# Kernel tuning notes

Measured on AMD Instinct MI355X. Metric: run time of the kernel, lower is better.

The kernel has to match this reference:

```python
import jax, jax.numpy as jnp
import numpy as np

EMBED, IN_DIM, HID, LAYERS, NVIEW = 1024, 256, 256, 3, 6


def _lstm_layer(x_seq, Wih, Whh, bih, bhh):
    # x_seq: [BM, N, D]; torch LSTM gate order i,f,g,o
    BM = x_seq.shape[0]
    h0 = jnp.zeros((BM, HID), x_seq.dtype)
    c0 = jnp.zeros((BM, HID), x_seq.dtype)

    def step(carry, x_t):
        h, c = carry
        gates = x_t @ Wih.T + bih + h @ Whh.T + bhh  # [BM, 4H]
        i, f, g, o = jnp.split(gates, 4, axis=-1)
        c = jax.nn.sigmoid(f) * c + jax.nn.sigmoid(i) * jnp.tanh(g)
        h = jax.nn.sigmoid(o) * jnp.tanh(c)
        return (h, c), h

    _, ys = jax.lax.scan(step, (h0, c0), jnp.swapaxes(x_seq, 0, 1))
    return jnp.swapaxes(ys, 0, 1)  # [BM, N, H]


def setup_inputs() -> dict:
    key = jax.random.key(0)
    ks = jax.random.split(key, 16)
    B, M = 32, 256
    s = lambda fan: 1.0 / np.sqrt(fan)
    inp = {
        "b_x_swin": jax.random.normal(ks[0], (B, M, NVIEW, EMBED), jnp.float32),
        "b_x_conv": jax.random.normal(ks[1], (B, M, NVIEW, EMBED), jnp.float32),
        "Wc": jax.random.uniform(ks[2], (EMBED, EMBED), jnp.float32, -s(EMBED), s(EMBED)),
        "bc": jax.random.uniform(ks[3], (EMBED,), jnp.float32, -s(EMBED), s(EMBED)),
        "Win": jax.random.uniform(ks[4], (IN_DIM, EMBED), jnp.float32, -s(EMBED), s(EMBED)),
        "b_in": jax.random.uniform(ks[5], (IN_DIM,), jnp.float32, -s(EMBED), s(EMBED)),
        "Wih": jax.random.uniform(ks[6], (LAYERS, 4 * HID, IN_DIM), jnp.float32, -s(HID), s(HID)),
        "Whh": jax.random.uniform(ks[7], (LAYERS, 4 * HID, HID), jnp.float32, -s(HID), s(HID)),
        "bih": jax.random.uniform(ks[8], (LAYERS, 4 * HID), jnp.float32, -s(HID), s(HID)),
        "bhh": jax.random.uniform(ks[9], (LAYERS, 4 * HID), jnp.float32, -s(HID), s(HID)),
        "Wv": jax.random.uniform(ks[10], (1, HID), jnp.float32, -s(HID), s(HID)),
        "bv": jax.random.uniform(ks[11], (1,), jnp.float32, -s(HID), s(HID)),
        "Ws": jax.random.uniform(ks[12], (1, NVIEW), jnp.float32, -s(NVIEW), s(NVIEW)),
        "bs": jax.random.uniform(ks[13], (1,), jnp.float32, -s(NVIEW), s(NVIEW)),
    }
    return inp


def reference(b_x_swin, b_x_conv, Wc, bc, Win, b_in, Wih, Whh, bih, bhh, Wv, bv, Ws, bs):
    B, M, N, C = b_x_swin.shape
    # fc_conv + exact GELU + residual (vectorized over all samples; same math as per-sample loop)
    x = b_x_swin + jax.nn.gelu(b_x_conv @ Wc.T + bc, approximate=False)
    x = x @ Win.T + b_in                         # [B, M, N, IN_DIM]
    x = x.reshape(B * M, N, IN_DIM)              # LSTM batch = B*M, seq = N
    for l in range(LAYERS):
        x = _lstm_layer(x, Wih[l], Whh[l], bih[l], bhh[l])
    v = (x @ Wv.T + bv).reshape(B, M, N)         # fc_viewport + flatten(1)
    score = (v @ Ws.T + bs).squeeze(-1)          # fc_score -> [B, M]
    return jnp.mean(score, axis=1)               # torch.mean per sample -> [B]
```

## Files before the change

### kernel.cpp

```cpp
#include <hip/hip_runtime.h>
#include <math.h>
#include <stdint.h>

typedef unsigned short u16;
typedef float f32x4 __attribute__((ext_vector_type(4)));
typedef short bf16x8 __attribute__((ext_vector_type(8)));

#define NVIEW 6

__device__ __forceinline__ u16 f2bf(float f){
  unsigned u = __float_as_uint(f);
  u += 0x7FFFu + ((u >> 16) & 1u);
  return (u16)(u >> 16);
}
__device__ __forceinline__ float bf2f(u16 h){
  return __uint_as_float(((unsigned)h) << 16);
}
__device__ __forceinline__ float fsig(float x){
  x = fminf(fmaxf(x, -30.f), 30.f);
  return 1.0f / (1.0f + __expf(-x));
}
__device__ __forceinline__ float ftanh(float x){
  x = fminf(fmaxf(x, -15.f), 15.f);
  float e = __expf(2.0f * x);
  return (e - 1.0f) / (e + 1.0f);
}
__device__ __forceinline__ void gload16(const u16* g, u16* l){
  __builtin_amdgcn_global_load_lds((const __attribute__((address_space(1))) unsigned int*)g,
                                   (__attribute__((address_space(3))) unsigned int*)l,
                                   16, 0, 0);
}

__global__ void k_cvt(const float* __restrict__ in, u16* __restrict__ out, long n4){
  long i = (long)blockIdx.x * blockDim.x + threadIdx.x;
  long stride = (long)gridDim.x * blockDim.x;
  for (; i < n4; i += stride){
    const float4 v = ((const float4*)in)[i];
    ushort4 o;
    o.x = f2bf(v.x); o.y = f2bf(v.y); o.z = f2bf(v.z); o.w = f2bf(v.w);
    ((ushort4*)out)[i] = o;
  }
}

__global__ void k_build_wl(const float* __restrict__ Wih, const float* __restrict__ Whh,
                           u16* __restrict__ Wl){
  int idx = blockIdx.x * 256 + threadIdx.x;
  int l   = idx >> 19;
  int rem = idx & 524287;
  int ro  = rem >> 9;
  int k   = rem & 511;
  int u = ro >> 2, q = ro & 3;
  int ri = q * 256 + u;
  float v = (k < 256) ? Wih[(l * 1024 + ri) * 256 + k]
                      : Whh[(l * 1024 + ri) * 256 + (k - 256)];
  Wl[idx] = f2bf(v);
}

__global__ void k_build_bias(const float* __restrict__ bih, const float* __restrict__ bhh,
                             float* __restrict__ biasL, u16* __restrict__ zbuf){
  int idx = blockIdx.x * 256 + threadIdx.x;
  if (idx < 3072){
    int l = idx >> 10; int ro = idx & 1023;
    int u = ro >> 2, q = ro & 3;
    int ri = q * 256 + u;
    biasL[idx] = bih[l * 1024 + ri] + bhh[l * 1024 + ri];
  }
  if (idx < 256) zbuf[idx] = 0;
}

#define DSR(dst, addr) asm volatile("ds_read_b128 %0, %1" : "=v"(dst) : "v"(addr))
#define VM4 asm volatile("s_waitcnt vmcnt(4)" ::: "memory")
#define VM0 asm volatile("s_waitcnt vmcnt(0)" ::: "memory")

template<int EPI>
__global__ __launch_bounds__(512, 2)
void gemm8p(const u16* __restrict__ A, long sA,
            const u16* __restrict__ Bm, long sB,
            int N, int K,
            const float* __restrict__ bias,
            const float* __restrict__ resid,
            u16* __restrict__ outb)
{
  __shared__ __align__(128) u16 shA[2 * 16384];
  __shared__ __align__(128) u16 shB[2 * 16384];

  const int tid  = threadIdx.x;
  const int lane = tid & 63;
  const int wv   = tid >> 6;
  const int wm   = wv >> 2;
  const int wn   = wv & 3;
  const int wm16 = wm * 16, wn16 = wn * 16;
  const int l15  = lane & 15, lk = lane >> 4;
  const int w2   = wv * 2;

  const int nwg = gridDim.x;
  const int qq  = nwg >> 3;
  const int b   = blockIdx.x;
  const int swz = (b & 7) * qq + (b >> 3);
  const int NB  = N >> 8;
  const long m0 = (long)(swz / NB) * 256;
  const int  n0 = (swz % NB) * 256;

  const int NT  = K >> 6;
  const int NIT = NT >> 1;

  const long laneA = (long)(lane >> 3) * sA + (long)(((lane & 7) ^ (lane >> 3)) << 3);
  const long laneB = (long)(lane >> 3) * sB + (long)(((lane & 7) ^ (lane >> 3)) << 3);

  auto STA = [&](int buf, int mh, int t){
    #pragma unroll
    for (int j = 0; j < 2; ++j){
      const int chunk = w2 + j;
      gload16(A + (m0 + mh * 128 + chunk * 8) * sA + (long)t * 64 + laneA,
              shA + buf * 16384 + mh * 8192 + chunk * 512 + lane * 8);
    }
  };
  auto STB = [&](int buf, int nh, int t){
    #pragma unroll
    for (int j = 0; j < 2; ++j){
      const int chunk = w2 + j;
      gload16(Bm + (long)(n0 + nh * 128 + chunk * 8) * sB + (long)t * 64 + laneB,
              shB + buf * 16384 + nh * 8192 + chunk * 512 + lane * 8);
    }
  };

  const unsigned ldsA = (unsigned)(uintptr_t)&shA[0];
  const unsigned ldsB = (unsigned)(uintptr_t)&shB[0];
  const unsigned aAr  = ldsA + (unsigned)((wm16 + l15) * 128 + ((lk ^ (l15 & 7)) << 4));
  const unsigned aBr  = ldsB + (unsigned)((wn16 + l15) * 128 + ((lk ^ (l15 & 7)) << 4));

  f32x4 acc[8][4];
  #pragma unroll
  for (int i = 0; i < 8; ++i)
    #pragma unroll
    for (int j = 0; j < 4; ++j)
      acc[i][j] = (f32x4){0.f, 0.f, 0.f, 0.f};

  STA(0, 0, 0); STB(0, 0, 0); STA(0, 1, 0); STB(0, 1, 0);
  STA(1, 0, 1); STB(1, 1, 1);
  VM4;
  __builtin_amdgcn_s_barrier();

#define PH(BUF, MH, NH, STG, VM)                                              \
  {                                                                           \
    bf16x8 af[2][4], bq[2][2];                                                \
    const unsigned bA  = aAr + ((BUF) * 32768 + (MH) * 16384);                \
    const unsigned bAx = bA ^ 64;                                             \
    const unsigned bB  = aBr + ((BUF) * 32768 + (NH) * 16384);                \
    const unsigned bBx = bB ^ 64;                                             \
    _Pragma("unroll") for (int i = 0; i < 4; ++i){                            \
      DSR(af[0][i], bA  + i * 4096);                                          \
      DSR(af[1][i], bAx + i * 4096);                                          \
    }                                                                         \
    _Pragma("unroll") for (int j = 0; j < 2; ++j){                            \
      DSR(bq[0][j], bB  + j * 8192);                                          \
      DSR(bq[1][j], bBx + j * 8192);                                          \
    }                                                                         \
    STG;                                                                      \
    __builtin_amdgcn_s_barrier();                                             \
    asm volatile("s_waitcnt lgkmcnt(0)" ::: "memory");                        \
    __builtin_amdgcn_sched_barrier(0);     \
    __builtin_amdgcn_s_setprio(1);                                            \
    _Pragma("unroll") for (int i = 0; i < 4; ++i)                             \
      _Pragma("unroll") for (int j = 0; j < 2; ++j)                           \
        _Pragma("unroll") for (int ks = 0; ks < 2; ++ks)                      \
          acc[(MH)*4 + i][(NH)*2 + j] = __builtin_amdgcn_mfma_f32_16x16x32_bf16( \
              af[ks][i], bq[ks][j], acc[(MH)*4 + i][(NH)*2 + j], 0, 0, 0);    \
    __builtin_amdgcn_s_setprio(0);                                            \
    VM;                                                                       \
    __builtin_amdgcn_s_barrier();                                             \
  }

  for (int it = 0; it < NIT - 1; ++it){
    const int t1 = 2 * it + 1;
    PH(0, 0, 0, STB(1, 0, t1),     (void)0);
    PH(0, 1, 0, STA(1, 1, t1),     (void)0);
    PH(0, 0, 1, STB(0, 0, t1 + 1), (void)0);
    PH(0, 1, 1, STA(0, 0, t1 + 1), VM4);
    PH(1, 0, 0, STA(0, 1, t1 + 1), (void)0);
    PH(1, 0, 1, STB(0, 1, t1 + 1), (void)0);
    PH(1, 1, 1, STA(1, 0, t1 + 2), (void)0);
    PH(1, 1, 0, STB(1, 1, t1 + 2), VM4);
  }
  {
    const int t1 = NT - 1;
    PH(0, 0, 0, STB(1, 0, t1), (void)0);
    PH(0, 1, 0, STA(1, 1, t1), (void)0);
    PH(0, 0, 1, (void)0,       (void)0);
    PH(0, 1, 1, (void)0,       VM0);
    PH(1, 0, 0, (void)0,       (void)0);
    PH(1, 0, 1, (void)0,       (void)0);
    PH(1, 1, 1, (void)0,       (void)0);
    PH(1, 1, 0, (void)0,       (void)0);
  }
#undef PH

  #pragma unroll
  for (int mf = 0; mf < 8; ++mf){
    #pragma unroll
    for (int nf = 0; nf < 4; ++nf){
      const int n = n0 + nf * 64 + wn16 + l15;
      const float bz = bias[n];
      const long mrow = m0 + mf * 32 + wm16 + lk * 4;
      #pragma unroll
      for (int r = 0; r < 4; ++r){
        float v = acc[mf][nf][r] + bz;
        const long off = (mrow + r) * (long)N + n;
        if (EPI == 0){
          float ge = 0.5f * v * (1.0f + erff(v * 0.70710678118654752f));
          v = ge + resid[off];
        }
        outb[off] = f2bf(v);
      }
    }
  }
}

template<int EPI>
__global__ __launch_bounds__(256)
void gemm_bt(const u16* __restrict__ A0, long sA0,
             const u16* __restrict__ A1, long sA1, int K0,
             const u16* __restrict__ Bm,
             int N, int K,
             const float* __restrict__ bias,
             const float* __restrict__ resid,
             u16* __restrict__ outb,
             float* __restrict__ cbuf,
             int tstep)
{
  __shared__ __align__(16) u16 lA[128 * 64];
  __shared__ __align__(16) u16 lB[128 * 64];

  const int tid  = threadIdx.x;
  const int lane = tid & 63;
  const int wid  = tid >> 6;
  const int wm = wid >> 1, wn = wid & 1;
  const int l15 = lane & 15, lk = lane >> 4;
  const long m0 = (long)blockIdx.x * 128;
  const int  n0 = blockIdx.y * 128;

  f32x4 acc[4][4];
  #pragma unroll
  for (int i = 0; i < 4; ++i)
    #pragma unroll
    for (int j = 0; j < 4; ++j)
      acc[i][j] = (f32x4){0.f, 0.f, 0.f, 0.f};

  const int rowL = tid >> 3;
  const int col8 = (tid & 7) * 8;

  for (int kt = 0; kt < (K >> 6); ++kt){
    const int kbase = kt << 6;
    #pragma unroll
    for (int c = 0; c < 4; ++c){
      int r = c * 32 + rowL;
      int k = kbase + col8;
      const u16* src = (k < K0) ? (A0 + (m0 + r) * sA0 + k)
                                : (A1 + (m0 + r) * sA1 + (k - K0));
      gload16(src, &lA[r * 64 + col8]);
    }
    #pragma unroll
    for (int c = 0; c < 4; ++c){
      int r = c * 32 + rowL;
      int k = kbase + col8;
      gload16(Bm + (long)(n0 + r) * K + k, &lB[r * 64 + col8]);
    }
    __syncthreads();

    #pragma unroll
    for (int ks = 0; ks < 2; ++ks){
      bf16x8 af[4], bfr[4];
      #pragma unroll
      for (int mf = 0; mf < 4; ++mf)
        af[mf] = *(const bf16x8*)&lA[(wm * 64 + mf * 16 + l15) * 64 + ks * 32 + lk * 8];
      #pragma unroll
      for (int nf = 0; nf < 4; ++nf)
        bfr[nf] = *(const bf16x8*)&lB[(wn * 64 + nf * 16 + l15) * 64 + ks * 32 + lk * 8];
      #pragma unroll
      for (int mf = 0; mf < 4; ++mf)
        #pragma unroll
        for (int nf = 0; nf < 4; ++nf)
          acc[mf][nf] = __builtin_amdgcn_mfma_f32_16x16x32_bf16(af[mf], bfr[nf], acc[mf][nf], 0, 0, 0);
    }
    __syncthreads();
  }

  if (EPI == 0 || EPI == 1){
    #pragma unroll
    for (int mf = 0; mf < 4; ++mf){
      #pragma unroll
      for (int nf = 0; nf < 4; ++nf){
        int  n    = n0 + wn * 64 + nf * 16 + l15;
        long mrow = m0 + wm * 64 + mf * 16 + lk * 4;
        float bz = bias[n];
        #pragma unroll
        for (int r = 0; r < 4; ++r){
          float v = acc[mf][nf][r] + bz;
          long off = (mrow + r) * N + n;
          if (EPI == 0){
            float ge = 0.5f * v * (1.0f + erff(v * 0.70710678118654752f));
            v = ge + resid[off];
          }
          outb[off] = f2bf(v);
        }
      }
    }
  } else {
    const int a  = lane & 3;
    const int qb = lane & ~3;
    #pragma unroll
    for (int mf = 0; mf < 4; ++mf){
      #pragma unroll
      for (int nf = 0; nf < 4; ++nf){
        int n = n0 + wn * 64 + nf * 16 + l15;
        float bz = bias[n];
        float v0 = acc[mf][nf][0] + bz;
        float v1 = acc[mf][nf][1] + bz;
        float v2 = acc[mf][nf][2] + bz;
        float v3 = acc[mf][nf][3] + bz;
        float s0 = (a == 0) ? v0 : (a == 1) ? v1 : (a == 2) ? v2 : v3;
        float s1 = (a == 0) ? v1 : (a == 1) ? v2 : (a == 2) ? v3 : v0;
        float s2 = (a == 0) ? v2 : (a == 1) ? v3 : (a == 2) ? v0 : v1;
        float s3 = (a == 0) ? v3 : (a == 1) ? v0 : (a == 2) ? v1 : v2;
        float r0 = s0;
        float r1 = __shfl(s1, qb + ((a + 3) & 3));
        float r2 = __shfl(s2, qb + ((a + 2) & 3));
        float r3 = __shfl(s3, qb + ((a + 1) & 3));
        float wi = (a == 0) ? r0 : (a == 1) ? r1 : (a == 2) ? r2 : r3;
        float wf = (a == 1) ? r0 : (a == 2) ? r1 : (a == 3) ? r2 : r3;
        float wg = (a == 2) ? r0 : (a == 3) ? r1 : (a == 0) ? r2 : r3;
        float wo = (a == 3) ? r0 : (a == 0) ? r1 : (a == 1) ? r2 : r3;
        long row = m0 + wm * 64 + mf * 16 + lk * 4 + a;
        int  u   = ((n0 + wn * 64 + nf * 16) >> 2) + (l15 >> 2);
        float c_old = (tstep == 0) ? 0.0f : cbuf[row * 256 + u];
        float ii = fsig(wi), ff = fsig(wf), gg = ftanh(wg), oo = fsig(wo);
        float cn = ff * c_old + ii * gg;
        float hn = oo * ftanh(cn);
        cbuf[row * 256 + u] = cn;
        outb[(row * NVIEW + tstep) * 256 + u] = f2bf(hn);
      }
    }
  }
}

__global__ void k_score(const u16* __restrict__ X3, const float* __restrict__ Wv,
                        const float* __restrict__ bv, const float* __restrict__ Ws,
                        const float* __restrict__ bs, float* __restrict__ score){
  int lane = threadIdx.x & 63;
  int bm = blockIdx.x * 4 + (threadIdx.x >> 6);
  const u16* row = X3 + (long)bm * (NVIEW * 256);
  float4 wv = *(const float4*)(Wv + lane * 4);
  float p = 0.f;
  #pragma unroll
  for (int n = 0; n < NVIEW; ++n){
    ushort4 xv = *(const ushort4*)(row + n * 256 + lane * 4);
    float d = bf2f(xv.x) * wv.x + bf2f(xv.y) * wv.y + bf2f(xv.z) * wv.z + bf2f(xv.w) * wv.w;
    p += Ws[n] * d;
  }
  #pragma unroll
  for (int off = 32; off; off >>= 1) p += __shfl_xor(p, off);
  if (lane == 0){
    float sw = Ws[0] + Ws[1] + Ws[2] + Ws[3] + Ws[4] + Ws[5];
    score[bm] = p + bv[0] * sw + bs[0];
  }
}

__global__ void k_mean(const float* __restrict__ score, float* __restrict__ out){
  __shared__ float red[256];
  int b = blockIdx.x, tid = threadIdx.x;
  red[tid] = score[b * 256 + tid];
  __syncthreads();
  for (int s = 128; s > 0; s >>= 1){
    if (tid < s) red[tid] += red[tid + s];
    __syncthreads();
  }
  if (tid == 0) out[b] = red[0] * (1.0f / 256.0f);
}

extern "C" void kernel_launch(void* const* d_in, const int* in_sizes, int n_in,
                              void* d_out, int out_size, void* d_ws, size_t ws_size,
                              hipStream_t stream){
  const float* swin = (const float*)d_in[0];
  const float* conv = (const float*)d_in[1];
  const float* Wc   = (const float*)d_in[2];
  const float* bc   = (const float*)d_in[3];
  const float* Win  = (const float*)d_in[4];
  const float* b_in = (const float*)d_in[5];
  const float* Wih  = (const float*)d_in[6];
  const float* Whh  = (const float*)d_in[7];
  const float* bih  = (const float*)d_in[8];
  const float* bhh  = (const float*)d_in[9];
  const float* Wv   = (const float*)d_in[10];
  const float* bv   = (const float*)d_in[11];
  const float* Ws   = (const float*)d_in[12];
  const float* bs   = (const float*)d_in[13];
  float* out = (float*)d_out;

  char* w = (char*)d_ws;
  u16*  convb = (u16*)(w);
  u16*  X0    = (u16*)(w);
  u16*  XA    = (u16*)(w + 25165824);
  u16*  XB    = (u16*)(w + 50331648);
  float* cbuf = (float*)(w + 75497472);
  u16*  Y     = (u16*)(w + 100663296);
  u16*  Wcb   = (u16*)(w + 201326592);
  u16*  Winb  = (u16*)(w + 203423744);
  u16*  Wl    = (u16*)(w + 203948032);
  float* biasL= (float*)(w + 207093760);
  u16*  zbuf  = (u16*)(w + 207106048);
  float* scoreb = (float*)(w + 207106560);

  k_cvt<<<4096, 256, 0, stream>>>(conv, convb, 49152L * 1024 / 4);
  k_cvt<<<512, 256, 0, stream>>>(Wc, Wcb, 1048576 / 4);
  k_cvt<<<128, 256, 0, stream>>>(Win, Winb, 262144 / 4);
  k_build_wl<<<6144, 256, 0, stream>>>(Wih, Whh, Wl);
  k_build_bias<<<12, 256, 0, stream>>>(bih, bhh, biasL, zbuf);

  gemm8p<0><<<768, 512, 0, stream>>>(convb, 1024L, Wcb, 1024L,
                                     1024, 1024, bc, swin, Y);

  gemm8p<1><<<192, 512, 0, stream>>>(Y, 1024L, Winb, 1024L,
                                     256, 1024, b_in, (const float*)nullptr, X0);

  const u16* xin = X0;
  u16* xout = XA;
  for (int l = 0; l < 3; ++l){
    for (int t = 0; t < 6; ++t){
      const u16* a1 = (t == 0) ? zbuf : (xout + (t - 1) * 256);
      long s1 = (t == 0) ? 0L : 1536L;
      gemm_bt<2><<<dim3(64, 8), 256, 0, stream>>>(
          xin + t * 256, 1536L, a1, s1, 256,
          Wl + l * 1024 * 512, 1024, 512,
          biasL + l * 1024, (const float*)nullptr,
          xout, cbuf, t);
    }
    if (l == 0){ xin = XA; xout = XB; }
    else if (l == 1){ xin = XB; xout = XA; }
  }

  k_score<<<2048, 256, 0, stream>>>(XA, Wv, bv, Ws, bs, scoreb);
  k_mean<<<32, 256, 0, stream>>>(scoreb, out);
}
```

Before: 857.6 us.

## Replace 8-phase interleaved GEMM pipeline with simple double-buffered K loop

Replaces the 8-phase ping-pong schedule, which split each 256x256 tile into quarter phases with staggered partial loads and barriers, with a plain double-buffered loop. Each iteration waits for all global loads, takes one barrier, prefetches the next K tile, reads all LDS fragments, and issues 64 MFMAs in two halves. This cuts the number of barriers and waitcnt points per K step. In exchange it loses the fine-grained overlap of loads with compute, and the full vmcnt(0) wait each iteration may expose memory latency.

```diff
diff --git a/kernel.cpp b/kernel.cpp
--- a/kernel.cpp
+++ b/kernel.cpp
@@ -69,12 +69,10 @@
 }
 
 #define DSR(dst, addr) asm volatile("ds_read_b128 %0, %1" : "=v"(dst) : "v"(addr))
-#define VM4 asm volatile("s_waitcnt vmcnt(4)" ::: "memory")
-#define VM0 asm volatile("s_waitcnt vmcnt(0)" ::: "memory")
 
 template<int EPI>
 __global__ __launch_bounds__(512, 2)
-void gemm8p(const u16* __restrict__ A, long sA,
+void gemm2p(const u16* __restrict__ A, long sA,
             const u16* __restrict__ Bm, long sB,
             int N, int K,
             const float* __restrict__ bias,
@@ -101,33 +99,34 @@
   const long m0 = (long)(swz / NB) * 256;
   const int  n0 = (swz % NB) * 256;
 
-  const int NT  = K >> 6;
-  const int NIT = NT >> 1;
+  const int NT = K >> 6;
 
   const long laneA = (long)(lane >> 3) * sA + (long)(((lane & 7) ^ (lane >> 3)) << 3);
   const long laneB = (long)(lane >> 3) * sB + (long)(((lane & 7) ^ (lane >> 3)) << 3);
 
-  auto STA = [&](int buf, int mh, int t){
-    #pragma unroll
-    for (int j = 0; j < 2; ++j){
-      const int chunk = w2 + j;
-      gload16(A + (m0 + mh * 128 + chunk * 8) * sA + (long)t * 64 + laneA,
-              shA + buf * 16384 + mh * 8192 + chunk * 512 + lane * 8);
-    }
-  };
-  auto STB = [&](int buf, int nh, int t){
-    #pragma unroll
-    for (int j = 0; j < 2; ++j){
-      const int chunk = w2 + j;
-      gload16(Bm + (long)(n0 + nh * 128 + chunk * 8) * sB + (long)t * 64 + laneB,
-              shB + buf * 16384 + nh * 8192 + chunk * 512 + lane * 8);
-    }
+  auto STAGE = [&](int buf, int t){
+    #pragma unroll
+    for (int mh = 0; mh < 2; ++mh)
+      #pragma unroll
+      for (int j = 0; j < 2; ++j){
+        const int chunk = w2 + j;
+        gload16(A + (m0 + mh * 128 + chunk * 8) * sA + (long)t * 64 + laneA,
+                shA + buf * 16384 + mh * 8192 + chunk * 512 + lane * 8);
+      }
+    #pragma unroll
+    for (int nh = 0; nh < 2; ++nh)
+      #pragma unroll
+      for (int j = 0; j < 2; ++j){
+        const int chunk = w2 + j;
+        gload16(Bm + (long)(n0 + nh * 128 + chunk * 8) * sB + (long)t * 64 + laneB,
+                shB + buf * 16384 + nh * 8192 + chunk * 512 + lane * 8);
+      }
   };
 
   const unsigned ldsA = (unsigned)(uintptr_t)&shA[0];
   const unsigned ldsB = (unsigned)(uintptr_t)&shB[0];
-  const unsigned aAr  = ldsA + (unsigned)((wm16 + l15) * 128 + ((lk ^ (l15 & 7)) << 4));
-  const unsigned aBr  = ldsB + (unsigned)((wn16 + l15) * 128 + ((lk ^ (l15 & 7)) << 4));
+  const unsigned aA0  = ldsA + (unsigned)((wm16 + l15) * 128 + ((lk ^ (l15 & 7)) << 4));
+  const unsigned aB0  = ldsB + (unsigned)((wn16 + l15) * 128 + ((lk ^ (l15 & 7)) << 4));
 
   f32x4 acc[8][4];
   #pragma unroll
@@ -136,64 +135,46 @@
     for (int j = 0; j < 4; ++j)
       acc[i][j] = (f32x4){0.f, 0.f, 0.f, 0.f};
 
-  STA(0, 0, 0); STB(0, 0, 0); STA(0, 1, 0); STB(0, 1, 0);
-  STA(1, 0, 1); STB(1, 1, 1);
-  VM4;
-  __builtin_amdgcn_s_barrier();
-
-#define PH(BUF, MH, NH, STG, VM)                                              \
-  {                                                                           \
-    bf16x8 af[2][4], bq[2][2];                                                \
-    const unsigned bA  = aAr + ((BUF) * 32768 + (MH) * 16384);                \
-    const unsigned bAx = bA ^ 64;                                             \
-    const unsigned bB  = aBr + ((BUF) * 32768 + (NH) * 16384);                \
-    const unsigned bBx = bB ^ 64;                                             \
-    _Pragma("unroll") for (int i = 0; i < 4; ++i){                            \
-      DSR(af[0][i], bA  + i * 4096);                                          \
-      DSR(af[1][i], bAx + i * 4096);                                          \
-    }                                                                         \
-    _Pragma("unroll") for (int j = 0; j < 2; ++j){                            \
-      DSR(bq[0][j], bB  + j * 8192);                                          \
-      DSR(bq[1][j], bBx + j * 8192);                                          \
-    }                                                                         \
-    STG;                                                                      \
-    __builtin_amdgcn_s_barrier();                                             \
-    asm volatile("s_waitcnt lgkmcnt(0)" ::: "memory");                        \
-    __builtin_amdgcn_sched_barrier(0);     \
-    __builtin_amdgcn_s_setprio(1);                                            \
-    _Pragma("unroll") for (int i = 0; i < 4; ++i)                             \
-      _Pragma("unroll") for (int j = 0; j < 2; ++j)                           \
-        _Pragma("unroll") for (int ks = 0; ks < 2; ++ks)                      \
-          acc[(MH)*4 + i][(NH)*2 + j] = __builtin_amdgcn_mfma_f32_16x16x32_bf16( \
-              af[ks][i], bq[ks][j], acc[(MH)*4 + i][(NH)*2 + j], 0, 0, 0);    \
-    __builtin_amdgcn_s_setprio(0);                                            \
-    VM;                                                                       \
-    __builtin_amdgcn_s_barrier();                                             \
-  }
-
-  for (int it = 0; it < NIT - 1; ++it){
-    const int t1 = 2 * it + 1;
-    PH(0, 0, 0, STB(1, 0, t1),     (void)0);
-    PH(0, 1, 0, STA(1, 1, t1),     (void)0);
-    PH(0, 0, 1, STB(0, 0, t1 + 1), (void)0);
-    PH(0, 1, 1, STA(0, 0, t1 + 1), VM4);
-    PH(1, 0, 0, STA(0, 1, t1 + 1), (void)0);
-    PH(1, 0, 1, STB(0, 1, t1 + 1), (void)0);
-    PH(1, 1, 1, STA(1, 0, t1 + 2), (void)0);
-    PH(1, 1, 0, STB(1, 1, t1 + 2), VM4);
-  }
-  {
-    const int t1 = NT - 1;
-    PH(0, 0, 0, STB(1, 0, t1), (void)0);
-    PH(0, 1, 0, STA(1, 1, t1), (void)0);
-    PH(0, 0, 1, (void)0,       (void)0);
-    PH(0, 1, 1, (void)0,       VM0);
-    PH(1, 0, 0, (void)0,       (void)0);
-    PH(1, 0, 1, (void)0,       (void)0);
-    PH(1, 1, 1, (void)0,       (void)0);
-    PH(1, 1, 0, (void)0,       (void)0);
-  }
-#undef PH
+  STAGE(0, 0);
+
+  for (int t = 0; t < NT; ++t){
+    const int cur = t & 1;
+    asm volatile("s_waitcnt vmcnt(0)" ::: "memory");
+    __builtin_amdgcn_s_barrier();
+    if (t + 1 < NT) STAGE(cur ^ 1, t + 1);
+
+    bf16x8 af[2][8], bq[2][4];
+    const unsigned bufOff = (unsigned)(cur * 32768);
+    const unsigned aA = aA0 + bufOff, aB = aB0 + bufOff;
+    #pragma unroll
+    for (int mf = 0; mf < 8; ++mf) DSR(af[0][mf], aA + mf * 4096);
+    #pragma unroll
+    for (int nf = 0; nf < 4; ++nf) DSR(bq[0][nf], aB + nf * 8192);
+    #pragma unroll
+    for (int mf = 0; mf < 8; ++mf) DSR(af[1][mf], (aA ^ 64) + mf * 4096);
+    #pragma unroll
+    for (int nf = 0; nf < 4; ++nf) DSR(bq[1][nf], (aB ^ 64) + nf * 8192);
+
+    asm volatile("s_waitcnt lgkmcnt(12)" ::: "memory");
+    __builtin_amdgcn_sched_barrier(0);
+    __builtin_amdgcn_s_setprio(1);
+    #pragma unroll
+    for (int mf = 0; mf < 8; ++mf)
+      #pragma unroll
+      for (int nf = 0; nf < 4; ++nf)
+        acc[mf][nf] = __builtin_amdgcn_mfma_f32_16x16x32_bf16(af[0][mf], bq[0][nf], acc[mf][nf], 0, 0, 0);
+    __builtin_amdgcn_s_setprio(0);
+
+    asm volatile("s_waitcnt lgkmcnt(0)" ::: "memory");
+    __builtin_amdgcn_sched_barrier(0);
+    __builtin_amdgcn_s_setprio(1);
+    #pragma unroll
+    for (int mf = 0; mf < 8; ++mf)
+      #pragma unroll
+      for (int nf = 0; nf < 4; ++nf)
+        acc[mf][nf] = __builtin_amdgcn_mfma_f32_16x16x32_bf16(af[1][mf], bq[1][nf], acc[mf][nf], 0, 0, 0);
+    __builtin_amdgcn_s_setprio(0);
+  }
 
   #pragma unroll
   for (int mf = 0; mf < 8; ++mf){
@@ -416,10 +397,10 @@
   k_build_wl<<<6144, 256, 0, stream>>>(Wih, Whh, Wl);
   k_build_bias<<<12, 256, 0, stream>>>(bih, bhh, biasL, zbuf);
 
-  gemm8p<0><<<768, 512, 0, stream>>>(convb, 1024L, Wcb, 1024L,
+  gemm2p<0><<<768, 512, 0, stream>>>(convb, 1024L, Wcb, 1024L,
                                      1024, 1024, bc, swin, Y);
 
-  gemm8p<1><<<192, 512, 0, stream>>>(Y, 1024L, Winb, 1024L,
+  gemm2p<1><<<192, 512, 0, stream>>>(Y, 1024L, Winb, 1024L,
                                      256, 1024, b_in, (const float*)nullptr, X0);
 
   const u16* xin = X0;
```

After: 831.7 us. 1.03x faster.
